# Performance work log

Measured on AMD Instinct MI355X. Metric: run time of the kernel, lower is better.

Reference implementation:

```python
import jax, jax.numpy as jnp
import numpy as np

E4M3_MAX = 448.0
MARGIN_FACTOR = 2.0  # margin=1 -> 2**1


def _fp8_scale(t):
    amax = jnp.max(jnp.abs(t))
    scale = E4M3_MAX / (amax * MARGIN_FACTOR + 1e-12)
    return jnp.clip(scale, 1e-12, 1e12)


def _quantize_e4m3_sim(t, scale):
    # simulated E4M3: clamp then round to 1/8 grid (module's non-native fallback)
    s = jnp.clip(t * scale, -E4M3_MAX, E4M3_MAX)
    return jnp.round(s * 8.0) / 8.0


def setup_inputs() -> dict:
    key = jax.random.key(0)
    k1, k2 = jax.random.split(key)
    M, IN, OUT = 32768, 1024, 1024
    x = jax.random.normal(k1, (M, IN), dtype=jnp.float32)
    weight_master = jax.random.normal(k2, (OUT, IN), dtype=jnp.float32) * (1.0 / np.sqrt(IN))
    bias = jnp.zeros((OUT,), dtype=jnp.float32)
    return {"x": x, "weight_master": weight_master, "bias": bias}


def reference(x, weight_master, bias):
    # weight quantization (done at init / sync_weights)
    w_scale = _fp8_scale(weight_master)
    w_fp8 = _quantize_e4m3_sim(weight_master, w_scale)
    # per-call dynamic activation scale + quantize
    a_scale = _fp8_scale(x)
    x_fp8 = _quantize_e4m3_sim(x, a_scale)
    # dequantize and GEMM (fp8_forward_dequant path)
    x_deq = x_fp8 / a_scale
    w_deq = w_fp8 / w_scale
    out = jnp.einsum('mk,nk->mn', x_deq, w_deq) + bias
    return out
```

## Files before the change

### kernel.cpp

```cpp
#include <hip/hip_runtime.h>
#include <hip/hip_bf16.h>
#include <hip/hip_fp16.h>

typedef _Float16 half8 __attribute__((ext_vector_type(8)));
typedef float f32x4 __attribute__((ext_vector_type(4)));

#define GM 32768
#define GN 1024
#define GK 1024

#define BM 256
#define BN 256
#define BK 32
#define NT (GK / BK)
#define SLOT_BYTES 32768
#define B_OFF 16384
#define A_HALF 8192
#define LDS_BYTES (3 * SLOT_BYTES)

#define AX_BLOCKS 2048
#define AW_BLOCKS 64
#define QX_BLOCKS 16384
#define QW_BLOCKS 512

__device__ __forceinline__ float fp8_scale_from_amax(float amax) {
    float s = 448.0f / (amax * 2.0f + 1e-12f);
    return fminf(fmaxf(s, 1e-12f), 1e12f);
}

__global__ __launch_bounds__(256) void amax_kernel(const float4* __restrict__ x,
                                                   const float4* __restrict__ w,
                                                   float* __restrict__ px,
                                                   float* __restrict__ pw) {
    __shared__ float red[4];
    int b = blockIdx.x;
    const float4* src; float* dst; int nb, bl;
    if (b < AX_BLOCKS) { src = x; dst = px + b; nb = AX_BLOCKS; bl = b; }
    else               { src = w; dst = pw + (b - AX_BLOCKS); nb = AW_BLOCKS; bl = b - AX_BLOCKS; }
    const size_t stride = (size_t)nb * 256;
    const float4* p = src + (size_t)bl * 256 + threadIdx.x;
    float m0 = 0.f, m1 = 0.f, m2 = 0.f, m3 = 0.f;
    #pragma unroll
    for (int j = 0; j < 4; ++j) {
        float4 a = p[0];
        float4 c = p[stride];
        float4 d = p[2 * stride];
        float4 e = p[3 * stride];
        p += 4 * stride;
        m0 = fmaxf(m0, fmaxf(fmaxf(fabsf(a.x), fabsf(a.y)), fmaxf(fabsf(a.z), fabsf(a.w))));
        m1 = fmaxf(m1, fmaxf(fmaxf(fabsf(c.x), fabsf(c.y)), fmaxf(fabsf(c.z), fabsf(c.w))));
        m2 = fmaxf(m2, fmaxf(fmaxf(fabsf(d.x), fabsf(d.y)), fmaxf(fabsf(d.z), fabsf(d.w))));
        m3 = fmaxf(m3, fmaxf(fmaxf(fabsf(e.x), fabsf(e.y)), fmaxf(fabsf(e.z), fabsf(e.w))));
    }
    float m = fmaxf(fmaxf(m0, m1), fmaxf(m2, m3));
    #pragma unroll
    for (int off = 32; off; off >>= 1) m = fmaxf(m, __shfl_xor(m, off));
    const int lane = threadIdx.x & 63, wid = threadIdx.x >> 6;
    if (lane == 0) red[wid] = m;
    __syncthreads();
    if (threadIdx.x == 0)
        *dst = fmaxf(fmaxf(red[0], red[1]), fmaxf(red[2], red[3]));
}

__global__ __launch_bounds__(256) void reduce_kernel(const float* __restrict__ px,
                                                     const float* __restrict__ pw,
                                                     unsigned* __restrict__ amax_bits) {
    __shared__ float red[8];
    const int tid = threadIdx.x, lane = tid & 63, wid = tid >> 6;
    float mx = 0.f;
    for (int i = tid; i < AX_BLOCKS; i += 256) mx = fmaxf(mx, px[i]);
    #pragma unroll
    for (int off = 32; off; off >>= 1) mx = fmaxf(mx, __shfl_xor(mx, off));
    if (lane == 0) red[wid] = mx;
    float mw = (tid < AW_BLOCKS) ? pw[tid] : 0.f;
    #pragma unroll
    for (int off = 32; off; off >>= 1) mw = fmaxf(mw, __shfl_xor(mw, off));
    if (tid == 0) red[4] = mw;
    __syncthreads();
    if (tid == 0) {
        float a = fmaxf(fmaxf(red[0], red[1]), fmaxf(red[2], red[3]));
        amax_bits[0] = __float_as_uint(a);
        amax_bits[1] = __float_as_uint(red[4]);
    }
}

__global__ __launch_bounds__(256) void quant_kernel(const float* __restrict__ x,
                                                    const float* __restrict__ w,
                                                    _Float16* __restrict__ X8,
                                                    _Float16* __restrict__ W8,
                                                    const unsigned* __restrict__ amax_bits) {
    int b = blockIdx.x;
    const float* src; _Float16* dst; int bl; int slot;
    if (b < QX_BLOCKS) { src = x; dst = X8; bl = b; slot = 0; }
    else               { src = w; dst = W8; bl = b - QX_BLOCKS; slot = 1; }
    float amax  = __uint_as_float(amax_bits[slot]);
    float scale = fp8_scale_from_amax(amax);
    size_t base = ((size_t)bl * 256 + threadIdx.x) * 8;
    float4 v0 = *(const float4*)(src + base);
    float4 v1 = *(const float4*)(src + base + 4);
    float vs[8] = {v0.x, v0.y, v0.z, v0.w, v1.x, v1.y, v1.z, v1.w};
    half8 h;
    #pragma unroll
    for (int j = 0; j < 8; ++j) {
        float s = vs[j] * scale;
        s = fminf(fmaxf(s, -448.0f), 448.0f);
        h[j] = (_Float16)rintf(s * 8.0f);
    }
    *(half8*)(dst + base) = h;
}

__global__ __launch_bounds__(512, 2) void gemm_kernel(const _Float16* __restrict__ A,
                                                      const _Float16* __restrict__ B,
                                                      const float* __restrict__ bias,
                                                      float* __restrict__ C,
                                                      const unsigned* __restrict__ amax_bits) {
    extern __shared__ char lds[];

    const int tid  = threadIdx.x;
    const int wid  = tid >> 6;
    const int lane = tid & 63;
    const int wr   = wid >> 2;
    const int wc   = wid & 3;
    const int l16  = lane & 15;
    const int kq   = lane >> 4;

    const int bid = blockIdx.x;
    const int swz = (bid & 7) * 64 + (bid >> 3);
    const int bm  = swz >> 2;
    const int bn  = swz & 3;
    const int row0 = bm * BM, col0 = bn * BN;

    const int rho  = tid >> 2;
    const int kap  = tid & 3;
    const int coff = ((kap ^ ((rho >> 1) & 3)) << 3);
    const _Float16* sA0 = A + (size_t)(row0 + rho) * GK + coff;
    const _Float16* sA1 = A + (size_t)(row0 + 128 + rho) * GK + coff;
    const _Float16* sB0 = B + (size_t)(col0 + rho) * GK + coff;
    const _Float16* sB1 = B + (size_t)(col0 + 128 + rho) * GK + coff;
    const int dA0 = wid * 1024;
    const int dA1 = A_HALF + wid * 1024;
    const int dB0 = B_OFF + wid * 1024;
    const int dB1 = B_OFF + A_HALF + wid * 1024;

    const int rsw  = kq ^ ((l16 >> 1) & 3);
    const int offA = (wr * 128 + l16) * 64 + (rsw << 4);
    const int offB = B_OFF + (wc * 64 + l16) * 64 + (rsw << 4);

    f32x4 acc[8][4] = {};

#define STAGE(slotidx) do {                                                            \
    char* sb_ = lds + (slotidx) * SLOT_BYTES;                                          \
    __builtin_amdgcn_global_load_lds((const __attribute__((address_space(1))) void*)sA0, \
        (__attribute__((address_space(3))) void*)(sb_ + dA0), 16, 0, 0);               \
    __builtin_amdgcn_global_load_lds((const __attribute__((address_space(1))) void*)sA1, \
        (__attribute__((address_space(3))) void*)(sb_ + dA1), 16, 0, 0);               \
    __builtin_amdgcn_global_load_lds((const __attribute__((address_space(1))) void*)sB0, \
        (__attribute__((address_space(3))) void*)(sb_ + dB0), 16, 0, 0);               \
    __builtin_amdgcn_global_load_lds((const __attribute__((address_space(1))) void*)sB1, \
        (__attribute__((address_space(3))) void*)(sb_ + dB1), 16, 0, 0);               \
    sA0 += BK; sA1 += BK; sB0 += BK; sB1 += BK;                                        \
} while (0)

#define MM(f, av)                                                                  \
    acc[f][0] = __builtin_amdgcn_mfma_f32_16x16x32_f16(av, bf0, acc[f][0], 0, 0, 0); \
    acc[f][1] = __builtin_amdgcn_mfma_f32_16x16x32_f16(av, bf1, acc[f][1], 0, 0, 0); \
    acc[f][2] = __builtin_amdgcn_mfma_f32_16x16x32_f16(av, bf2, acc[f][2], 0, 0, 0); \
    acc[f][3] = __builtin_amdgcn_mfma_f32_16x16x32_f16(av, bf3, acc[f][3], 0, 0, 0);

#define COMPUTE(slotidx) do {                                  \
    const char* cb_ = lds + (slotidx) * SLOT_BYTES;            \
    half8 bf0 = *(const half8*)(cb_ + offB + 0 * 1024);        \
    half8 bf1 = *(const half8*)(cb_ + offB + 1 * 1024);        \
    half8 bf2 = *(const half8*)(cb_ + offB + 2 * 1024);        \
    half8 bf3 = *(const half8*)(cb_ + offB + 3 * 1024);        \
    half8 a0 = *(const half8*)(cb_ + offA + 0 * 1024);         \
    half8 a1 = *(const half8*)(cb_ + offA + 1 * 1024);         \
    half8 a2 = *(const half8*)(cb_ + offA + 2 * 1024);         \
    half8 a3 = *(const half8*)(cb_ + offA + 3 * 1024);         \
    __builtin_amdgcn_s_setprio(1);                             \
    MM(0, a0) MM(1, a1) MM(2, a2) MM(3, a3)                    \
    __builtin_amdgcn_s_setprio(0);                             \
    half8 a4 = *(const half8*)(cb_ + offA + 4 * 1024);         \
    half8 a5 = *(const half8*)(cb_ + offA + 5 * 1024);         \
    half8 a6 = *(const half8*)(cb_ + offA + 6 * 1024);         \
    half8 a7 = *(const half8*)(cb_ + offA + 7 * 1024);         \
    __builtin_amdgcn_s_setprio(1);                             \
    MM(4, a4) MM(5, a5) MM(6, a6) MM(7, a7)                    \
    __builtin_amdgcn_s_setprio(0);                             \
} while (0)

    STAGE(0);
    STAGE(1);
    for (int t = 0; t < NT; ++t) {
        if (t < NT - 1) { asm volatile("s_waitcnt vmcnt(4)" ::: "memory"); }
        else            { asm volatile("s_waitcnt vmcnt(0)" ::: "memory"); }
        __builtin_amdgcn_s_barrier();
        asm volatile("" ::: "memory");
        if (t + 2 < NT) STAGE((t + 2) % 3);
        COMPUTE(t % 3);
    }

#undef STAGE
#undef COMPUTE
#undef MM

    float sa = fp8_scale_from_amax(__uint_as_float(amax_bits[0]));
    float sw = fp8_scale_from_amax(__uint_as_float(amax_bits[1]));
    float rs = 1.0f / (64.0f * sa * sw);

    const int orow = row0 + wr * 128 + kq * 4;
    const int ocol = col0 + wc * 64 + l16;
    float bvv[4];
    #pragma unroll
    for (int n = 0; n < 4; ++n) bvv[n] = bias[ocol + n * 16];
    #pragma unroll
    for (int f = 0; f < 8; ++f) {
        #pragma unroll
        for (int n = 0; n < 4; ++n) {
            const int cc = ocol + n * 16;
            #pragma unroll
            for (int i = 0; i < 4; ++i) {
                const int rr = orow + f * 16 + i;
                C[(size_t)rr * GN + cc] = acc[f][n][i] * rs + bvv[n];
            }
        }
    }
}

extern "C" void kernel_launch(void* const* d_in, const int* in_sizes, int n_in,
                              void* d_out, int out_size, void* d_ws, size_t ws_size,
                              hipStream_t stream) {
    const float* x    = (const float*)d_in[0];
    const float* w    = (const float*)d_in[1];
    const float* bias = (const float*)d_in[2];
    float* out        = (float*)d_out;

    unsigned* amax_bits = (unsigned*)d_ws;
    float* px = (float*)((char*)d_ws + 4096);
    float* pw = px + AX_BLOCKS;
    _Float16* X8 = (_Float16*)((char*)d_ws + 65536);
    _Float16* W8 = (_Float16*)((char*)d_ws + 65536 + (size_t)GM * GK * 2);

    amax_kernel<<<AX_BLOCKS + AW_BLOCKS, 256, 0, stream>>>(
        (const float4*)x, (const float4*)w, px, pw);

    reduce_kernel<<<1, 256, 0, stream>>>(px, pw, amax_bits);

    quant_kernel<<<QX_BLOCKS + QW_BLOCKS, 256, 0, stream>>>(x, w, X8, W8, amax_bits);

    (void)hipFuncSetAttribute((const void*)gemm_kernel,
                              hipFuncAttributeMaxDynamicSharedMemorySize, LDS_BYTES);
    gemm_kernel<<<(GM / BM) * (GN / BN), 512, LDS_BYTES, stream>>>(X8, W8, bias, out, amax_bits);
}
```

Baseline: 331.9 us.

## Restructure GEMM main loop into fine-grained 8-phase ping-pong pipeline

Replaces the 3-slot BK=32 pipeline with a double-buffered BK=64 layout split into half-tiles. Each loop iteration is unrolled into eight phases, and each phase interleaves LDS reads, one async global-to-LDS stage and a 16-MFMA cluster between barriers. The goal is to overlap memory traffic with MFMA work more evenly and to amortize the per-tile barrier and waitcnt cost. In exchange there are more barriers, a larger 128KB LDS footprint, and the last tiles are reloaded redundantly through clamped indices.

```diff
diff --git a/kernel.cpp b/kernel.cpp
--- a/kernel.cpp
+++ b/kernel.cpp
@@ -8,15 +8,10 @@
 #define GM 32768
 #define GN 1024
 #define GK 1024
-
-#define BM 256
-#define BN 256
-#define BK 32
-#define NT (GK / BK)
-#define SLOT_BYTES 32768
-#define B_OFF 16384
-#define A_HALF 8192
-#define LDS_BYTES (3 * SLOT_BYTES)
+#define NKT 16
+#define NIT 8
+
+#define LDS_BYTES 131072
 
 #define AX_BLOCKS 2048
 #define AW_BLOCKS 64
@@ -128,81 +123,94 @@
     const int swz = (bid & 7) * 64 + (bid >> 3);
     const int bm  = swz >> 2;
     const int bn  = swz & 3;
-    const int row0 = bm * BM, col0 = bn * BN;
-
-    const int rho  = tid >> 2;
-    const int kap  = tid & 3;
-    const int coff = ((kap ^ ((rho >> 1) & 3)) << 3);
-    const _Float16* sA0 = A + (size_t)(row0 + rho) * GK + coff;
-    const _Float16* sA1 = A + (size_t)(row0 + 128 + rho) * GK + coff;
-    const _Float16* sB0 = B + (size_t)(col0 + rho) * GK + coff;
-    const _Float16* sB1 = B + (size_t)(col0 + 128 + rho) * GK + coff;
-    const int dA0 = wid * 1024;
-    const int dA1 = A_HALF + wid * 1024;
-    const int dB0 = B_OFF + wid * 1024;
-    const int dB1 = B_OFF + A_HALF + wid * 1024;
-
-    const int rsw  = kq ^ ((l16 >> 1) & 3);
-    const int offA = (wr * 128 + l16) * 64 + (rsw << 4);
-    const int offB = B_OFF + (wc * 64 + l16) * 64 + (rsw << 4);
+    const int row0 = bm * 256, col0 = bn * 256;
+
+    const int r    = tid >> 2;
+    const int ch   = tid & 3;
+    const int kl   = ch ^ ((r >> 1) & 3);
+    const _Float16* gA = A + (size_t)(row0 + r) * GK + kl * 8;
+    const _Float16* gB = B + (size_t)(col0 + r) * GK + kl * 8;
+    const int dstoff = wid * 1024;
+
+    const int rsw  = (kq ^ ((l16 >> 1) & 3)) << 4;
+    const int aoff = (wr * 128 + l16) * 64 + rsw;
+    const int boff = (wc * 64 + l16) * 64 + rsw;
 
     f32x4 acc[8][4] = {};
-
-#define STAGE(slotidx) do {                                                            \
-    char* sb_ = lds + (slotidx) * SLOT_BYTES;                                          \
-    __builtin_amdgcn_global_load_lds((const __attribute__((address_space(1))) void*)sA0, \
-        (__attribute__((address_space(3))) void*)(sb_ + dA0), 16, 0, 0);               \
-    __builtin_amdgcn_global_load_lds((const __attribute__((address_space(1))) void*)sA1, \
-        (__attribute__((address_space(3))) void*)(sb_ + dA1), 16, 0, 0);               \
-    __builtin_amdgcn_global_load_lds((const __attribute__((address_space(1))) void*)sB0, \
-        (__attribute__((address_space(3))) void*)(sb_ + dB0), 16, 0, 0);               \
-    __builtin_amdgcn_global_load_lds((const __attribute__((address_space(1))) void*)sB1, \
-        (__attribute__((address_space(3))) void*)(sb_ + dB1), 16, 0, 0);               \
-    sA0 += BK; sA1 += BK; sB0 += BK; sB1 += BK;                                        \
+    half8 bf0, bf1, bf2, bf3, a0, a1, a2, a3;
+
+#define STAGE(d, T, kh, kt, g) do {                                                     \
+    const _Float16* s_ = (g) + (size_t)(kt) * 64 + (kh) * 32;                           \
+    char* dst_ = lds + (d) * 65536 + (T) * 32768 + (kh) * 16384 + dstoff;               \
+    __builtin_amdgcn_global_load_lds((const __attribute__((address_space(1))) void*)s_, \
+        (__attribute__((address_space(3))) void*)dst_, 16, 0, 0);                       \
+    __builtin_amdgcn_global_load_lds(                                                   \
+        (const __attribute__((address_space(1))) void*)(s_ + (size_t)128 * GK),         \
+        (__attribute__((address_space(3))) void*)(dst_ + 8192), 16, 0, 0);              \
 } while (0)
 
-#define MM(f, av)                                                                  \
-    acc[f][0] = __builtin_amdgcn_mfma_f32_16x16x32_f16(av, bf0, acc[f][0], 0, 0, 0); \
-    acc[f][1] = __builtin_amdgcn_mfma_f32_16x16x32_f16(av, bf1, acc[f][1], 0, 0, 0); \
-    acc[f][2] = __builtin_amdgcn_mfma_f32_16x16x32_f16(av, bf2, acc[f][2], 0, 0, 0); \
+#define RD_B(d, ks) do { const char* p_ = lds + (d) * 65536 + 32768 + (ks) * 16384;     \
+    bf0 = *(const half8*)(p_ + boff);        bf1 = *(const half8*)(p_ + boff + 1024);   \
+    bf2 = *(const half8*)(p_ + boff + 2048); bf3 = *(const half8*)(p_ + boff + 3072); } while (0)
+
+#define RD_A(d, ks, mh) do { const char* p_ = lds + (d) * 65536 + (ks) * 16384 + (mh) * 4096; \
+    a0 = *(const half8*)(p_ + aoff);         a1 = *(const half8*)(p_ + aoff + 1024);    \
+    a2 = *(const half8*)(p_ + aoff + 2048);  a3 = *(const half8*)(p_ + aoff + 3072); } while (0)
+
+#define MM4(f, av)                                                                      \
+    acc[f][0] = __builtin_amdgcn_mfma_f32_16x16x32_f16(av, bf0, acc[f][0], 0, 0, 0);    \
+    acc[f][1] = __builtin_amdgcn_mfma_f32_16x16x32_f16(av, bf1, acc[f][1], 0, 0, 0);    \
+    acc[f][2] = __builtin_amdgcn_mfma_f32_16x16x32_f16(av, bf2, acc[f][2], 0, 0, 0);    \
     acc[f][3] = __builtin_amdgcn_mfma_f32_16x16x32_f16(av, bf3, acc[f][3], 0, 0, 0);
 
-#define COMPUTE(slotidx) do {                                  \
-    const char* cb_ = lds + (slotidx) * SLOT_BYTES;            \
-    half8 bf0 = *(const half8*)(cb_ + offB + 0 * 1024);        \
-    half8 bf1 = *(const half8*)(cb_ + offB + 1 * 1024);        \
-    half8 bf2 = *(const half8*)(cb_ + offB + 2 * 1024);        \
-    half8 bf3 = *(const half8*)(cb_ + offB + 3 * 1024);        \
-    half8 a0 = *(const half8*)(cb_ + offA + 0 * 1024);         \
-    half8 a1 = *(const half8*)(cb_ + offA + 1 * 1024);         \
-    half8 a2 = *(const half8*)(cb_ + offA + 2 * 1024);         \
-    half8 a3 = *(const half8*)(cb_ + offA + 3 * 1024);         \
-    __builtin_amdgcn_s_setprio(1);                             \
-    MM(0, a0) MM(1, a1) MM(2, a2) MM(3, a3)                    \
-    __builtin_amdgcn_s_setprio(0);                             \
-    half8 a4 = *(const half8*)(cb_ + offA + 4 * 1024);         \
-    half8 a5 = *(const half8*)(cb_ + offA + 5 * 1024);         \
-    half8 a6 = *(const half8*)(cb_ + offA + 6 * 1024);         \
-    half8 a7 = *(const half8*)(cb_ + offA + 7 * 1024);         \
-    __builtin_amdgcn_s_setprio(1);                             \
-    MM(4, a4) MM(5, a5) MM(6, a6) MM(7, a7)                    \
-    __builtin_amdgcn_s_setprio(0);                             \
-} while (0)
-
-    STAGE(0);
-    STAGE(1);
-    for (int t = 0; t < NT; ++t) {
-        if (t < NT - 1) { asm volatile("s_waitcnt vmcnt(4)" ::: "memory"); }
-        else            { asm volatile("s_waitcnt vmcnt(0)" ::: "memory"); }
-        __builtin_amdgcn_s_barrier();
-        asm volatile("" ::: "memory");
-        if (t + 2 < NT) STAGE((t + 2) % 3);
-        COMPUTE(t % 3);
+#define MFMA16(mh) do { __builtin_amdgcn_s_setprio(1);                                  \
+    MM4((mh) * 4 + 0, a0) MM4((mh) * 4 + 1, a1)                                         \
+    MM4((mh) * 4 + 2, a2) MM4((mh) * 4 + 3, a3)                                         \
+    __builtin_amdgcn_s_setprio(0); } while (0)
+
+#define BAR() do { asm volatile("" ::: "memory"); __builtin_amdgcn_s_barrier();         \
+                   asm volatile("" ::: "memory"); } while (0)
+#define CKPT() asm volatile("s_waitcnt vmcnt(6)" ::: "memory")
+
+    STAGE(0, 1, 0, 0, gB);
+    STAGE(0, 0, 0, 0, gA);
+    STAGE(0, 1, 1, 0, gB);
+    STAGE(0, 0, 1, 0, gA);
+    STAGE(1, 1, 0, 1, gB);
+    STAGE(1, 0, 0, 1, gA);
+    STAGE(1, 1, 1, 1, gB);
+    CKPT();
+    BAR();
+
+    for (int j = 0; j < NIT; ++j) {
+        const int kt1 = 2 * j + 1;
+        const int kn0 = (2 * j + 2 < NKT - 1) ? 2 * j + 2 : NKT - 1;
+        const int kn1 = (2 * j + 3 < NKT - 1) ? 2 * j + 3 : NKT - 1;
+        RD_B(0, 0); RD_A(0, 0, 0); STAGE(1, 0, 1, kt1, gA);
+        BAR(); MFMA16(0); BAR();
+        RD_A(0, 0, 1); STAGE(0, 1, 0, kn0, gB);
+        BAR(); MFMA16(1); BAR();
+        RD_B(0, 1); RD_A(0, 1, 0); STAGE(0, 0, 0, kn0, gA);
+        BAR(); MFMA16(0); BAR();
+        RD_A(0, 1, 1); STAGE(0, 1, 1, kn0, gB); CKPT();
+        BAR(); MFMA16(1); BAR();
+        RD_B(1, 0); RD_A(1, 0, 0); STAGE(0, 0, 1, kn0, gA);
+        BAR(); MFMA16(0); BAR();
+        RD_A(1, 0, 1); STAGE(1, 1, 0, kn1, gB);
+        BAR(); MFMA16(1); BAR();
+        RD_B(1, 1); RD_A(1, 1, 0); STAGE(1, 0, 0, kn1, gA);
+        BAR(); MFMA16(0); BAR();
+        RD_A(1, 1, 1); STAGE(1, 1, 1, kn1, gB); CKPT();
+        BAR(); MFMA16(1); BAR();
     }
 
 #undef STAGE
-#undef COMPUTE
-#undef MM
+#undef RD_B
+#undef RD_A
+#undef MM4
+#undef MFMA16
+#undef BAR
+#undef CKPT
 
     float sa = fp8_scale_from_amax(__uint_as_float(amax_bits[0]));
     float sw = fp8_scale_from_amax(__uint_as_float(amax_bits[1]));
@@ -250,5 +258,5 @@
 
     (void)hipFuncSetAttribute((const void*)gemm_kernel,
                               hipFuncAttributeMaxDynamicSharedMemorySize, LDS_BYTES);
-    gemm_kernel<<<(GM / BM) * (GN / BN), 512, LDS_BYTES, stream>>>(X8, W8, bias, out, amax_bits);
-}
+    gemm_kernel<<<(GM / 256) * (GN / 256), 512, LDS_BYTES, stream>>>(X8, W8, bias, out, amax_bits);
+}
```

Result: no change. 332.3 us (+0.1%).
